# Performance work log

Measured on AMD Instinct MI355X. Metric: run time of the kernel, lower is better.

Reference implementation:

```python
import jax, jax.numpy as jnp
import numpy as np

N, D_IN, D_OUT = 16384, 1024, 1024
E, R, TOP_K = 8, 16, 2
ALPHA = 32.0
SCALING = ALPHA / R  # standard LoRA scaling alpha/rank


def setup_inputs() -> dict:
    key = jax.random.key(0)
    k_tok, k_wb, k_a, k_b, k_g = jax.random.split(key, 5)
    tokens = jax.random.normal(k_tok, (N, D_IN), dtype=jnp.float32)
    # frozen attention projection
    W_base = jax.random.normal(k_wb, (D_IN, D_OUT), dtype=jnp.float32) * (1.0 / np.sqrt(D_IN))
    # per-expert LoRA factors
    A = jax.random.normal(k_a, (E, D_IN, R), dtype=jnp.float32) * 0.02
    B = jax.random.normal(k_b, (E, R, D_OUT), dtype=jnp.float32) * 0.02
    # router
    W_gate = jax.random.normal(k_g, (D_IN, E), dtype=jnp.float32) * (1.0 / np.sqrt(D_IN))
    return {"tokens": tokens, "W_base": W_base, "A": A, "B": B, "W_gate": W_gate}


def reference(tokens, W_base, A, B, W_gate):
    # Router: top-k gating with softmax over the selected logits
    router_logits = tokens @ W_gate                      # [N, E]
    topk_vals, selected_experts = jax.lax.top_k(router_logits, TOP_K)  # [N, K]
    expert_weights = jax.nn.softmax(topk_vals, axis=-1)  # [N, K]

    # Dense combine weights: zeros except selected experts
    gates = jnp.zeros((tokens.shape[0], E), dtype=tokens.dtype)
    gates = gates.at[jnp.arange(tokens.shape[0])[:, None], selected_experts].set(expert_weights)  # [N, E]

    # Frozen base projection
    base_out = tokens @ W_base                           # [N, D_out]

    # LoRA experts: low-rank intermediate [N, E, R] is small (rank 16)
    h = jnp.einsum('nd,edr->ner', tokens, A)             # [N, E, R]
    h = h * gates[:, :, None]                            # gate before expanding to D_out
    lora_out = jnp.einsum('ner,erm->nm', h, B)           # [N, D_out]

    out = base_out + SCALING * lora_out
    return out, router_logits, selected_experts, expert_weights
```

## Files before the change

kernel.cpp:

```cpp
#include <hip/hip_runtime.h>
#include <hip/hip_bf16.h>
#include <cstdint>
#include <cfloat>

#define NTOK 16384
#define DIN  1024
#define DOUT 1024
#define NEXP 8
#define RLORA 16
#define KTOT 1152
#define SCALE_LORA 2.0f

typedef __attribute__((ext_vector_type(8))) short bf16x8;
typedef __attribute__((ext_vector_type(4))) float f32x4;

__device__ __forceinline__ unsigned short f2bf(float f) {
  __hip_bfloat16 h = __float2bfloat16(f);
  unsigned short u;
  __builtin_memcpy(&u, &h, 2);
  return u;
}

__device__ __forceinline__ void gld_lds16(const void* g, void* l) {
  __builtin_amdgcn_global_load_lds((const __attribute__((address_space(1))) void*)g,
                                   (__attribute__((address_space(3))) void*)l,
                                   16, 0, 0);
}

__global__ __launch_bounds__(256) void k_prep(const float* __restrict__ Wb,
                                              const float* __restrict__ B,
                                              const float* __restrict__ A,
                                              const float* __restrict__ Wg,
                                              unsigned short* __restrict__ WcatT,
                                              unsigned short* __restrict__ AcatT,
                                              float* __restrict__ WgT) {
  __shared__ unsigned short Tbuf[256 * 17];
  const int bid = blockIdx.x;
  const int t = threadIdx.x;
  if (bid < 288) {
    unsigned short (*T)[66] = (unsigned short (*)[66])Tbuf;
    const int k0 = (bid % 18) * 64, j0 = (bid / 18) * 64;
#pragma unroll
    for (int p = 0; p < 4; ++p) {
      int kk = p * 16 + (t >> 4);
      int c4 = (t & 15) * 4;
      int k = k0 + kk;
      const float* src = (k < 1024) ? (Wb + (size_t)k * 1024) : (B + (size_t)(k - 1024) * 1024);
      float4 v = *(const float4*)(src + j0 + c4);
      T[kk][c4 + 0] = f2bf(v.x); T[kk][c4 + 1] = f2bf(v.y);
      T[kk][c4 + 2] = f2bf(v.z); T[kk][c4 + 3] = f2bf(v.w);
    }
    __syncthreads();
#pragma unroll
    for (int p = 0; p < 2; ++p) {
      int jj = p * 32 + (t >> 3);
      int kc = (t & 7) * 8;
      unsigned short buf[8];
#pragma unroll
      for (int i = 0; i < 8; ++i) buf[i] = T[kc + i][jj];
      uint4 u; __builtin_memcpy(&u, buf, 16);
      *(uint4*)(WcatT + (size_t)(j0 + jj) * KTOT + k0 + kc) = u;
    }
  } else if (bid < 320) {
    unsigned short (*T)[17] = (unsigned short (*)[17])Tbuf;
    const int e = (bid - 288) >> 2, d0 = ((bid - 288) & 3) * 256;
#pragma unroll
    for (int p = 0; p < 4; ++p) {
      int idx = p * 256 + t;
      int d = idx >> 2;
      int rr = (idx & 3) * 4;
      float4 v = *(const float4*)(A + (size_t)e * 16384 + (size_t)(d0 + d) * 16 + rr);
      T[d][rr + 0] = f2bf(v.x); T[d][rr + 1] = f2bf(v.y);
      T[d][rr + 2] = f2bf(v.z); T[d][rr + 3] = f2bf(v.w);
    }
    __syncthreads();
#pragma unroll
    for (int p = 0; p < 2; ++p) {
      int slot = p * 256 + t;
      int r = slot >> 5;
      int dc = (slot & 31) * 8;
      unsigned short buf[8];
#pragma unroll
      for (int i = 0; i < 8; ++i) buf[i] = T[dc + i][r];
      uint4 u; __builtin_memcpy(&u, buf, 16);
      *(uint4*)(AcatT + (size_t)(e * 16 + r) * 1024 + d0 + dc) = u;
    }
  } else {
    int d = (bid - 320) * 256 + t;
    float4 a = *(const float4*)(Wg + (size_t)d * 8);
    float4 b = *(const float4*)(Wg + (size_t)d * 8 + 4);
    WgT[0 * 1024 + d] = a.x; WgT[1 * 1024 + d] = a.y;
    WgT[2 * 1024 + d] = a.z; WgT[3 * 1024 + d] = a.w;
    WgT[4 * 1024 + d] = b.x; WgT[5 * 1024 + d] = b.y;
    WgT[6 * 1024 + d] = b.z; WgT[7 * 1024 + d] = b.w;
  }
}

__global__ __launch_bounds__(256) void k_router(const float* __restrict__ tokens,
                                                const float* __restrict__ WgT,
                                                float* __restrict__ out_logits,
                                                float* __restrict__ out_sel,
                                                float* __restrict__ out_w,
                                                unsigned short* __restrict__ Xcat,
                                                float4* __restrict__ gateinfo) {
  const int wid = threadIdx.x >> 6;
  const int lane = threadIdx.x & 63;
  const int t0 = (blockIdx.x * 4 + wid) * 2;

  float4 xa[4], xb[4];
  const float* x0 = tokens + (size_t)t0 * DIN;
  const float* x1 = x0 + DIN;
#pragma unroll
  for (int j = 0; j < 4; ++j) {
    xa[j] = *(const float4*)(x0 + j * 256 + lane * 4);
    xb[j] = *(const float4*)(x1 + j * 256 + lane * 4);
  }

#pragma unroll
  for (int tt = 0; tt < 2; ++tt) {
    unsigned short* xbp = Xcat + (size_t)(t0 + tt) * KTOT;
    const float4* xv = tt ? xb : xa;
#pragma unroll
    for (int j = 0; j < 4; ++j) {
      const float* xf = (const float*)&xv[j];
      unsigned short hb[4];
#pragma unroll
      for (int m = 0; m < 4; ++m) hb[m] = f2bf(xf[m]);
      uint2 u;
      __builtin_memcpy(&u, hb, 8);
      *(uint2*)(xbp + j * 256 + lane * 4) = u;
    }
  }

  float accA[8] = {0,0,0,0,0,0,0,0}, accB[8] = {0,0,0,0,0,0,0,0};
#pragma unroll
  for (int j = 0; j < 4; ++j) {
#pragma unroll
    for (int e = 0; e < 8; ++e) {
      float4 wv = *(const float4*)(WgT + (size_t)e * 1024 + j * 256 + lane * 4);
      accA[e] = fmaf(xa[j].x, wv.x, fmaf(xa[j].y, wv.y,
                fmaf(xa[j].z, wv.z, fmaf(xa[j].w, wv.w, accA[e]))));
      accB[e] = fmaf(xb[j].x, wv.x, fmaf(xb[j].y, wv.y,
                fmaf(xb[j].z, wv.z, fmaf(xb[j].w, wv.w, accB[e]))));
    }
  }
#pragma unroll
  for (int s = 1; s < 64; s <<= 1) {
#pragma unroll
    for (int e = 0; e < 8; ++e) {
      accA[e] += __shfl_xor(accA[e], s, 64);
      accB[e] += __shfl_xor(accB[e], s, 64);
    }
  }

#pragma unroll
  for (int tt = 0; tt < 2; ++tt) {
    const float* acc = tt ? accB : accA;
    int t = t0 + tt;
    float v0 = -FLT_MAX, v1 = -FLT_MAX;
    int i0 = -1, i1 = -1;
#pragma unroll
    for (int e = 0; e < 8; ++e) {
      float v = acc[e];
      if (v > v0) { v1 = v0; i1 = i0; v0 = v; i0 = e; }
      else if (v > v1) { v1 = v; i1 = e; }
    }
    float ex = expf(v1 - v0);
    float inv = 1.0f / (1.0f + ex);
    float w0 = inv, w1 = ex * inv;
    if (lane == 0) {
      float4* lg = (float4*)(out_logits + (size_t)t * 8);
      lg[0] = make_float4(acc[0], acc[1], acc[2], acc[3]);
      lg[1] = make_float4(acc[4], acc[5], acc[6], acc[7]);
      *(float2*)(out_sel + (size_t)t * 2) = make_float2((float)i0, (float)i1);
      *(float2*)(out_w + (size_t)t * 2) = make_float2(w0, w1);
      gateinfo[t] = make_float4((float)i0, (float)i1, w0 * SCALE_LORA, w1 * SCALE_LORA);
    }
  }
}

__global__ __launch_bounds__(256) void k_hgemm(const unsigned short* __restrict__ Xg,
                                               const unsigned short* __restrict__ Ag,
                                               const float4* __restrict__ gateinfo,
                                               unsigned short* __restrict__ Xout) {
  constexpr int BK = 64;
  __shared__ alignas(16) unsigned short As[64 * BK];
  __shared__ alignas(16) unsigned short Bs[64 * BK];
  const int tid = threadIdx.x;
  const int lane = tid & 63;
  const int wid = tid >> 6;
  const int id = blockIdx.x;
  const int xcd = id & 7, s5 = id >> 3;
  const int n0 = (s5 & 1) * 64;
  const int m0 = (xcd * 32 + (s5 >> 1)) * 64;
  const int wm = (wid >> 1) * 32, wn = (wid & 1) * 32;
  const int quad = lane >> 4, r16 = lane & 15;

  f32x4 acc[2][2] = {};

  for (int k0 = 0; k0 < 1024; k0 += BK) {
#pragma unroll
    for (int i = 0; i < 2; ++i) {
      int s = i * 256 + tid;
      int r = s >> 3, c = s & 7;
      int q = c ^ ((r >> 1) & 7);
      gld_lds16(Xg + (size_t)(m0 + r) * KTOT + k0 + q * 8, (char*)As + s * 16);
    }
#pragma unroll
    for (int i = 0; i < 2; ++i) {
      int s = i * 256 + tid;
      int r = s >> 3, c = s & 7;
      int q = c ^ ((r >> 1) & 7);
      gld_lds16(Ag + (size_t)(n0 + r) * 1024 + k0 + q * 8, (char*)Bs + s * 16);
    }
    __syncthreads();

#pragma unroll
    for (int h = 0; h < 2; ++h) {
      bf16x8 af[2], bfr[2];
#pragma unroll
      for (int mi = 0; mi < 2; ++mi) {
        int m = wm + mi * 16 + r16;
        int slot = m * 8 + ((h * 4 + quad) ^ ((m >> 1) & 7));
        af[mi] = *(const bf16x8*)((const char*)As + slot * 16);
      }
#pragma unroll
      for (int ni = 0; ni < 2; ++ni) {
        int n = wn + ni * 16 + r16;
        int slot = n * 8 + ((h * 4 + quad) ^ ((n >> 1) & 7));
        bfr[ni] = *(const bf16x8*)((const char*)Bs + slot * 16);
      }
#pragma unroll
      for (int mi = 0; mi < 2; ++mi)
#pragma unroll
        for (int ni = 0; ni < 2; ++ni)
          acc[mi][ni] = __builtin_amdgcn_mfma_f32_16x16x32_bf16(af[mi], bfr[ni], acc[mi][ni], 0, 0, 0);
    }
    __syncthreads();
  }

#pragma unroll
  for (int mi = 0; mi < 2; ++mi)
#pragma unroll
    for (int r = 0; r < 4; ++r) {
      int row = m0 + wm + mi * 16 + quad * 4 + r;
      float4 gi = gateinfo[row];
      int ie0 = (int)gi.x, ie1 = (int)gi.y;
#pragma unroll
      for (int ni = 0; ni < 2; ++ni) {
        int c = n0 + wn + ni * 16 + r16;
        int e = c >> 4;
        float h = acc[mi][ni][r];
        float v = (e == ie0) ? gi.z * h : ((e == ie1) ? gi.w * h : 0.f);
        Xout[(size_t)row * KTOT + 1024 + c] = f2bf(v);
      }
    }
}

__global__ __launch_bounds__(256, 4) void k_gemm_main(const unsigned short* __restrict__ Xg,
                                                      const unsigned short* __restrict__ Wgm,
                                                      float* __restrict__ C) {
  __shared__ alignas(16) unsigned short As[128 * 64];
  __shared__ alignas(16) unsigned short Bs[128 * 64];
  const int tid = threadIdx.x;
  const int lane = tid & 63;
  const int wid = tid >> 6;
  const int id = blockIdx.x;
  const int gid = (id & 7) * 128 + (id >> 3);
  const int m0 = (gid >> 3) * 128;
  const int n0 = (gid & 7) * 128;
  const int wm = (wid >> 1) * 64, wn = (wid & 1) * 64;
  const int quad = lane >> 4, r16 = lane & 15;

  f32x4 acc[4][4] = {};

  for (int kt = 0; kt < 18; ++kt) {
    const int k0 = kt * 64;
#pragma unroll
    for (int i = 0; i < 4; ++i) {
      int s = i * 256 + tid;
      int r = s >> 3, c = s & 7;
      int q = c ^ ((r >> 1) & 7);
      gld_lds16(Xg + (size_t)(m0 + r) * KTOT + k0 + q * 8, (char*)As + s * 16);
    }
#pragma unroll
    for (int i = 0; i < 4; ++i) {
      int s = i * 256 + tid;
      int r = s >> 3, c = s & 7;
      int q = c ^ ((r >> 1) & 7);
      gld_lds16(Wgm + (size_t)(n0 + r) * KTOT + k0 + q * 8, (char*)Bs + s * 16);
    }
    __syncthreads();

#pragma unroll
    for (int h = 0; h < 2; ++h) {
      bf16x8 af[4], bfr[4];
#pragma unroll
      for (int mi = 0; mi < 4; ++mi) {
        int m = wm + mi * 16 + r16;
        int slot = m * 8 + ((h * 4 + quad) ^ ((m >> 1) & 7));
        af[mi] = *(const bf16x8*)((const char*)As + slot * 16);
      }
#pragma unroll
      for (int ni = 0; ni < 4; ++ni) {
        int n = wn + ni * 16 + r16;
        int slot = n * 8 + ((h * 4 + quad) ^ ((n >> 1) & 7));
        bfr[ni] = *(const bf16x8*)((const char*)Bs + slot * 16);
      }
#pragma unroll
      for (int mi = 0; mi < 4; ++mi)
#pragma unroll
        for (int ni = 0; ni < 4; ++ni)
          acc[mi][ni] = __builtin_amdgcn_mfma_f32_16x16x32_bf16(af[mi], bfr[ni], acc[mi][ni], 0, 0, 0);
    }
    __syncthreads();
  }

#pragma unroll
  for (int mi = 0; mi < 4; ++mi)
#pragma unroll
    for (int ni = 0; ni < 4; ++ni)
#pragma unroll
      for (int r = 0; r < 4; ++r) {
        int row = m0 + wm + mi * 16 + quad * 4 + r;
        int cc = n0 + wn + ni * 16 + r16;
        C[(size_t)row * 1024 + cc] = acc[mi][ni][r];
      }
}

extern "C" void kernel_launch(void* const* d_in, const int* in_sizes, int n_in,
                              void* d_out, int out_size, void* d_ws, size_t ws_size,
                              hipStream_t stream) {
  const float* tokens = (const float*)d_in[0];
  const float* Wb     = (const float*)d_in[1];
  const float* A      = (const float*)d_in[2];
  const float* B      = (const float*)d_in[3];
  const float* Wg     = (const float*)d_in[4];
  float* out = (float*)d_out;

  char* ws = (char*)d_ws;
  unsigned short* Xcat  = (unsigned short*)(ws);
  unsigned short* WcatT = (unsigned short*)(ws + 37748736);
  unsigned short* AcatT = (unsigned short*)(ws + 40108032);
  float4*         ginfo = (float4*)(ws + 40370176);
  float*          WgT   = (float*)(ws + 40632320);

  float* out_logits = out + (size_t)16384 * 1024;
  float* out_sel    = out_logits + (size_t)16384 * 8;
  float* out_w      = out_sel + (size_t)16384 * 2;

  k_prep<<<dim3(324), dim3(256), 0, stream>>>(Wb, B, A, Wg, WcatT, AcatT, WgT);
  k_router<<<dim3(2048), dim3(256), 0, stream>>>(tokens, WgT, out_logits, out_sel, out_w, Xcat, ginfo);
  k_hgemm<<<dim3(512), dim3(256), 0, stream>>>(Xcat, AcatT, ginfo, Xcat);
  k_gemm_main<<<dim3(1024), dim3(256), 0, stream>>>(Xcat, WcatT, out);
}
```

Before: 180.4 us.

## Double-buffer LDS tiles in LoRA h-GEMM kernel to overlap loads with MFMA

The k_hgemm kernel now keeps two LDS buffers per operand and issues the global-to-LDS loads for the next K tile before running the MFMAs on the current one. The old code loaded a tile, synchronised, then computed. This is meant to hide global load latency behind compute. It doubles LDS use per block and replaces __syncthreads with an explicit vmcnt wait plus s_barrier, which may hurt occupancy. Note that k_hgemm is only a small part of the total work, since the base GEMM dominates.

```diff
diff --git a/kernel.cpp b/kernel.cpp
--- a/kernel.cpp
+++ b/kernel.cpp
@@ -184,8 +184,8 @@
                                                const float4* __restrict__ gateinfo,
                                                unsigned short* __restrict__ Xout) {
   constexpr int BK = 64;
-  __shared__ alignas(16) unsigned short As[64 * BK];
-  __shared__ alignas(16) unsigned short Bs[64 * BK];
+  __shared__ alignas(16) unsigned short As[2][64 * BK];
+  __shared__ alignas(16) unsigned short Bs[2][64 * BK];
   const int tid = threadIdx.x;
   const int lane = tid & 63;
   const int wid = tid >> 6;
@@ -198,22 +198,34 @@
 
   f32x4 acc[2][2] = {};
 
-  for (int k0 = 0; k0 < 1024; k0 += BK) {
-#pragma unroll
-    for (int i = 0; i < 2; ++i) {
-      int s = i * 256 + tid;
-      int r = s >> 3, c = s & 7;
-      int q = c ^ ((r >> 1) & 7);
-      gld_lds16(Xg + (size_t)(m0 + r) * KTOT + k0 + q * 8, (char*)As + s * 16);
-    }
-#pragma unroll
-    for (int i = 0; i < 2; ++i) {
-      int s = i * 256 + tid;
-      int r = s >> 3, c = s & 7;
-      int q = c ^ ((r >> 1) & 7);
-      gld_lds16(Ag + (size_t)(n0 + r) * 1024 + k0 + q * 8, (char*)Bs + s * 16);
-    }
-    __syncthreads();
+#define HST(d, kt)                                                            \
+  {                                                                           \
+    const int k0s = (kt) * BK;                                                \
+    _Pragma("unroll")                                                         \
+    for (int i_ = 0; i_ < 2; ++i_) {                                          \
+      int s_ = i_ * 256 + tid;                                                \
+      int r_ = s_ >> 3, c_ = s_ & 7;                                          \
+      int q_ = c_ ^ ((r_ >> 1) & 7);                                          \
+      gld_lds16(Xg + (size_t)(m0 + r_) * KTOT + k0s + q_ * 8,                 \
+                (char*)As[d] + s_ * 16);                                      \
+    }                                                                         \
+    _Pragma("unroll")                                                         \
+    for (int i_ = 0; i_ < 2; ++i_) {                                          \
+      int s_ = i_ * 256 + tid;                                                \
+      int r_ = s_ >> 3, c_ = s_ & 7;                                          \
+      int q_ = c_ ^ ((r_ >> 1) & 7);                                          \
+      gld_lds16(Ag + (size_t)(n0 + r_) * 1024 + k0s + q_ * 8,                 \
+                (char*)Bs[d] + s_ * 16);                                      \
+    }                                                                         \
+  }
+
+  HST(0, 0);
+  asm volatile("s_waitcnt vmcnt(0)" ::: "memory");
+  __builtin_amdgcn_s_barrier();
+
+  int cur = 0;
+  for (int t = 0; t < 16; ++t) {
+    if (t < 15) HST(cur ^ 1, t + 1);
 
 #pragma unroll
     for (int h = 0; h < 2; ++h) {
@@ -222,13 +234,13 @@
       for (int mi = 0; mi < 2; ++mi) {
         int m = wm + mi * 16 + r16;
         int slot = m * 8 + ((h * 4 + quad) ^ ((m >> 1) & 7));
-        af[mi] = *(const bf16x8*)((const char*)As + slot * 16);
+        af[mi] = *(const bf16x8*)((const char*)As[cur] + slot * 16);
       }
 #pragma unroll
       for (int ni = 0; ni < 2; ++ni) {
         int n = wn + ni * 16 + r16;
         int slot = n * 8 + ((h * 4 + quad) ^ ((n >> 1) & 7));
-        bfr[ni] = *(const bf16x8*)((const char*)Bs + slot * 16);
+        bfr[ni] = *(const bf16x8*)((const char*)Bs[cur] + slot * 16);
       }
 #pragma unroll
       for (int mi = 0; mi < 2; ++mi)
@@ -236,8 +248,11 @@
         for (int ni = 0; ni < 2; ++ni)
           acc[mi][ni] = __builtin_amdgcn_mfma_f32_16x16x32_bf16(af[mi], bfr[ni], acc[mi][ni], 0, 0, 0);
     }
-    __syncthreads();
-  }
+    asm volatile("s_waitcnt vmcnt(0)" ::: "memory");
+    __builtin_amdgcn_s_barrier();
+    cur ^= 1;
+  }
+#undef HST
 
 #pragma unroll
   for (int mi = 0; mi < 2; ++mi)
```

New measurement: 184.4 us. +2.2%, slower.
